# Optimization experiments

Measured on AMD Instinct MI355X. Metric: run time of the kernel, lower is better.

The kernel has to match this reference:

```python
import jax, jax.numpy as jnp
import numpy as np

EPS = 1e-10  # matches torch float32 path


def setup_inputs() -> dict:
    key = jax.random.key(0)
    ks = jax.random.split(key, 8)
    B, E, D, N = 32, 32000, 128, 1000
    scale = 1.0 / np.sqrt(D)
    return {
        "edge_attr": jax.random.normal(ks[0], (B, E, D), dtype=jnp.float32),
        "edge_index": jax.random.randint(ks[1], (B, 2, E), 0, N, dtype=jnp.int64),
        "W1": jax.random.normal(ks[2], (D, D), dtype=jnp.float32) * scale,
        "b1": jax.random.normal(ks[3], (D,), dtype=jnp.float32) * 0.01,
        "W2": jax.random.normal(ks[4], (D, D), dtype=jnp.float32) * scale,
        "b2": jax.random.normal(ks[5], (D,), dtype=jnp.float32) * 0.01,
        "Wout": jax.random.normal(ks[6], (1, D), dtype=jnp.float32) * scale,
        "bout": jax.random.normal(ks[7], (1,), dtype=jnp.float32) * 0.01,
        "num_nodes": N,
    }


def reference(edge_attr, edge_index, W1, b1, W2, b2, Wout, bout, num_nodes):
    # Edge MLP: (num_layers-1)=2 hidden silu linears, then 1-dim sigmoid output
    x = jax.nn.silu(jnp.einsum("bed,fd->bef", edge_attr, W1) + b1)
    x = jax.nn.silu(jnp.einsum("bed,fd->bef", x, W2) + b2)
    vals = jax.nn.sigmoid(jnp.einsum("bed,od->beo", x, Wout) + bout)[..., 0]  # [B, E]
    B = vals.shape[0]
    b_idx = jnp.arange(B)[:, None]  # [B, 1] broadcasts over E
    heatmap = jnp.zeros((B, num_nodes, num_nodes), dtype=vals.dtype)
    heatmap = heatmap.at[b_idx, edge_index[:, 0], edge_index[:, 1]].set(vals)
    return jnp.log(heatmap + EPS)
```

## Files before the change

kernel.cpp:

```cpp
#include <hip/hip_runtime.h>
#include <stdint.h>
#include <string.h>
#include <math.h>

typedef float f32x4 __attribute__((ext_vector_type(4)));
typedef unsigned int u32;

#define DD 128

__device__ __forceinline__ float fsilu(float x) {
    float e = __expf(-x);
    return x * __builtin_amdgcn_rcpf(1.0f + e);
}
__device__ __forceinline__ u32 pk4fp8(float a, float b, float c, float d) {
    u32 r = __builtin_amdgcn_cvt_pk_fp8_f32(a, b, 0u, false);
    return __builtin_amdgcn_cvt_pk_fp8_f32(c, d, r, true);
}

__device__ __forceinline__ float decz(u32 u) {
    float z = (float)(int)(u & 0x3FFFu) * (1.0f / 256.0f) - 40.0f;
    float s = __builtin_amdgcn_rcpf(1.0f + __expf(-z));
    return __logf(s + 1e-10f);
}
__global__ void decode_sparse(u32* __restrict__ p, long n4, u32 le) {
    long i  = (long)blockIdx.x * blockDim.x + threadIdx.x;
    long st = (long)gridDim.x * blockDim.x;
    for (long k = i; k < n4; k += st) {
        uint4 u = ((const uint4*)p)[k];
        float* f = (float*)(p + k * 4);
        if (u.x >= 0xE0000000u) f[0] = decz(u.x); else if (u.x != le) ((u32*)f)[0] = le;
        if (u.y >= 0xE0000000u) f[1] = decz(u.y); else if (u.y != le) ((u32*)f)[1] = le;
        if (u.z >= 0xE0000000u) f[2] = decz(u.z); else if (u.z != le) ((u32*)f)[2] = le;
        if (u.w >= 0xE0000000u) f[3] = decz(u.w); else if (u.w != le) ((u32*)f)[3] = le;
    }
}

__global__ __launch_bounds__(1024)
void mlp_scatter(const float* __restrict__ A,
                 const int* __restrict__ eidx,
                 const float* __restrict__ W1, const float* __restrict__ B1,
                 const float* __restrict__ W2, const float* __restrict__ B2,
                 const float* __restrict__ WO, const float* __restrict__ BO,
                 u32* __restrict__ out,
                 int E, int nWT, int N)
{
    extern __shared__ char smem[];
    uint2* W1s = (uint2*)smem;
    uint2* W2s = (uint2*)(smem + 16384);
    float* b1s = (float*)(smem + 32768);
    float* b2s = (float*)(smem + 33280);
    float* wos = (float*)(smem + 33792);
    uint2* Hs  = (uint2*)(smem + 34304);

    const int tid  = threadIdx.x;
    const int lane = tid & 63;
    const int wave = tid >> 6;
    const int lrow = lane & 15;
    const int lg   = lane >> 4;

    #pragma unroll
    for (int c = 0; c < 2; ++c) {
        int id = c * 1024 + tid;
        int mt = id >> 8, kk = (id >> 6) & 3, ln = id & 63;
        const float* p1 = W1 + (mt * 16 + (ln & 15)) * DD + kk * 32 + (ln >> 4) * 8;
        const float* p2 = W2 + (mt * 16 + (ln & 15)) * DD + kk * 32 + (ln >> 4) * 8;
        float4 x0 = *(const float4*)p1, x1 = *(const float4*)(p1 + 4);
        float4 y0 = *(const float4*)p2, y1 = *(const float4*)(p2 + 4);
        W1s[mt * 256 + kk * 64 + ln] = make_uint2(pk4fp8(x0.x, x0.y, x0.z, x0.w),
                                                  pk4fp8(x1.x, x1.y, x1.z, x1.w));
        W2s[mt * 256 + kk * 64 + ln] = make_uint2(pk4fp8(y0.x, y0.y, y0.z, y0.w),
                                                  pk4fp8(y1.x, y1.y, y1.z, y1.w));
    }
    if (tid < DD) { b1s[tid] = B1[tid]; b2s[tid] = B2[tid]; wos[tid] = WO[tid]; }
    const float bo = BO[0];
    const size_t NN = (size_t)N * (size_t)N;
    uint2* HsW = Hs + wave * 256;
    __syncthreads();

    const int wid  = blockIdx.x * 16 + wave;
    const int step = (int)gridDim.x * 16;
    if (wid >= nWT) return;

    float4 va[8];
    {
        const float* Ar = A + (size_t)((wid << 4) + lrow) * DD;
        #pragma unroll
        for (int kk = 0; kk < 4; ++kk) {
            const float* p = Ar + kk * 32 + lg * 8;
            va[2 * kk]     = *(const float4*)p;
            va[2 * kk + 1] = *(const float4*)(p + 4);
        }
    }

    for (int wt = wid; wt < nWT; wt += step) {
        const int r0  = wt << 4;
        const int b   = r0 / E;
        const int ei0 = r0 - b * E;
        int i0 = 0, j0 = 0;
        if (lane < 16) {
            i0 = eidx[(size_t)(2 * b) * E + ei0 + lane];
            j0 = eidx[(size_t)(2 * b + 1) * E + ei0 + lane];
        }

        uint2 ef[4];
        #pragma unroll
        for (int kk = 0; kk < 4; ++kk)
            ef[kk] = make_uint2(
                pk4fp8(va[2*kk].x,   va[2*kk].y,   va[2*kk].z,   va[2*kk].w),
                pk4fp8(va[2*kk+1].x, va[2*kk+1].y, va[2*kk+1].z, va[2*kk+1].w));

        {
            int tn = wt + step; if (tn >= nWT) tn = wt;
            const float* Ar = A + (size_t)((tn << 4) + lrow) * DD;
            #pragma unroll
            for (int kk = 0; kk < 4; ++kk) {
                const float* p = Ar + kk * 32 + lg * 8;
                va[2 * kk]     = *(const float4*)p;
                va[2 * kk + 1] = *(const float4*)(p + 4);
            }
        }

        f32x4 acc[8];
        #pragma unroll
        for (int mt = 0; mt < 8; ++mt)
            acc[mt] = *(const f32x4*)&b1s[mt * 16 + lg * 4];
        #pragma unroll
        for (int kk = 0; kk < 4; ++kk)
            #pragma unroll
            for (int mt = 0; mt < 8; ++mt)
                acc[mt] = __builtin_amdgcn_mfma_f32_16x16x32_fp8_fp8(
                    __builtin_bit_cast(long, W1s[mt * 256 + kk * 64 + lane]),
                    __builtin_bit_cast(long, ef[kk]), acc[mt], 0, 0, 0);

        #pragma unroll
        for (int mt = 0; mt < 8; ++mt) {
            int lnp = (((mt & 1) << 1) | (lg >> 1)) * 16 + lrow;
            u32 pw = pk4fp8(fsilu(acc[mt][0]), fsilu(acc[mt][1]),
                            fsilu(acc[mt][2]), fsilu(acc[mt][3]));
            ((u32*)&HsW[(mt >> 1) * 64 + lnp])[lg & 1] = pw;
        }

        f32x4 acc2[8];
        #pragma unroll
        for (int mt = 0; mt < 8; ++mt)
            acc2[mt] = *(const f32x4*)&b2s[mt * 16 + lg * 4];
        #pragma unroll
        for (int kk = 0; kk < 4; ++kk) {
            long hf = __builtin_bit_cast(long, HsW[kk * 64 + lane]);
            #pragma unroll
            for (int mt = 0; mt < 8; ++mt)
                acc2[mt] = __builtin_amdgcn_mfma_f32_16x16x32_fp8_fp8(
                    __builtin_bit_cast(long, W2s[mt * 256 + kk * 64 + lane]),
                    hf, acc2[mt], 0, 0, 0);
        }

        float zp = 0.f;
        #pragma unroll
        for (int mt = 0; mt < 8; ++mt) {
            f32x4 w4 = *(const f32x4*)&wos[mt * 16 + lg * 4];
            zp += w4[0] * fsilu(acc2[mt][0]) + w4[1] * fsilu(acc2[mt][1])
                + w4[2] * fsilu(acc2[mt][2]) + w4[3] * fsilu(acc2[mt][3]);
        }
        zp += __shfl_xor(zp, 16);
        zp += __shfl_xor(zp, 32);

        if (lane < 16) {
            float z = zp + bo;
            int qz = (int)((z + 40.0f) * 256.0f + 0.5f);
            qz = qz < 0 ? 0 : (qz > 16383 ? 16383 : qz);
            u32 packed = 0xE0000000u | ((u32)(ei0 + lane + 1) << 14) | (u32)qz;
            atomicMax(&out[(size_t)b * NN + (size_t)i0 * N + (size_t)j0], packed);
        }
    }
}

extern "C" void kernel_launch(void* const* d_in, const int* in_sizes, int n_in,
                              void* d_out, int out_size, void* d_ws, size_t ws_size,
                              hipStream_t stream) {
    const float* edge_attr  = (const float*)d_in[0];
    const int*   edge_index = (const int*)d_in[1];
    const float* W1   = (const float*)d_in[2];
    const float* b1   = (const float*)d_in[3];
    const float* W2   = (const float*)d_in[4];
    const float* b2   = (const float*)d_in[5];
    const float* Wout = (const float*)d_in[6];
    const float* bout = (const float*)d_in[7];

    long rows = (long)in_sizes[0] / DD;
    int  E    = in_sizes[1] / 64;
    int  nWT  = (int)(rows / 16);
    int  Bb   = (int)(rows / E);
    int  N    = (int)(sqrtf((float)(out_size / Bb)) + 0.5f);

    u32* outp = (u32*)d_out;
    long n4 = (long)out_size >> 2;

    float fv = logf(1e-10f);
    u32 LE; memcpy(&LE, &fv, 4);

    const int SMEM = 67072;
    hipFuncSetAttribute((const void*)mlp_scatter,
                        hipFuncAttributeMaxDynamicSharedMemorySize, SMEM);

    mlp_scatter<<<256, 1024, SMEM, stream>>>(edge_attr, edge_index, W1, b1, W2, b2,
                                             Wout, bout, outp, E, nWT, N);
    decode_sparse<<<2048, 256, 0, stream>>>(outp, n4, LE);
}
```

Before: 179.7 us.

## Shrink MLP blocks to 512 threads, drop register prefetch, reuse accumulators

Moves the fused MLP-scatter kernel from 256 blocks of 1024 threads to 768 blocks of 512 threads, cutting shared memory per block so more blocks can be resident per CU. It removes the software prefetch of the next tile's edge features held in registers and loads and packs the current tile directly. It also reuses the first-layer accumulator array for the second layer. The aim is lower register pressure and more waves in flight to hide memory latency, at the cost of exposing load latency that the prefetch used to hide and doing the weight staging more times across the larger grid.

```diff
diff --git a/kernel.cpp b/kernel.cpp
--- a/kernel.cpp
+++ b/kernel.cpp
@@ -35,7 +35,7 @@
     }
 }
 
-__global__ __launch_bounds__(1024)
+__global__ __launch_bounds__(512)
 void mlp_scatter(const float* __restrict__ A,
                  const int* __restrict__ eidx,
                  const float* __restrict__ W1, const float* __restrict__ B1,
@@ -59,8 +59,8 @@
     const int lg   = lane >> 4;
 
     #pragma unroll
-    for (int c = 0; c < 2; ++c) {
-        int id = c * 1024 + tid;
+    for (int c = 0; c < 4; ++c) {
+        int id = c * 512 + tid;
         int mt = id >> 8, kk = (id >> 6) & 3, ln = id & 63;
         const float* p1 = W1 + (mt * 16 + (ln & 15)) * DD + kk * 32 + (ln >> 4) * 8;
         const float* p2 = W2 + (mt * 16 + (ln & 15)) * DD + kk * 32 + (ln >> 4) * 8;
@@ -77,20 +77,8 @@
     uint2* HsW = Hs + wave * 256;
     __syncthreads();
 
-    const int wid  = blockIdx.x * 16 + wave;
-    const int step = (int)gridDim.x * 16;
-    if (wid >= nWT) return;
-
-    float4 va[8];
-    {
-        const float* Ar = A + (size_t)((wid << 4) + lrow) * DD;
-        #pragma unroll
-        for (int kk = 0; kk < 4; ++kk) {
-            const float* p = Ar + kk * 32 + lg * 8;
-            va[2 * kk]     = *(const float4*)p;
-            va[2 * kk + 1] = *(const float4*)(p + 4);
-        }
-    }
+    const int wid  = blockIdx.x * 8 + wave;
+    const int step = (int)gridDim.x * 8;
 
     for (int wt = wid; wt < nWT; wt += step) {
         const int r0  = wt << 4;
@@ -103,21 +91,24 @@
         }
 
         uint2 ef[4];
-        #pragma unroll
-        for (int kk = 0; kk < 4; ++kk)
-            ef[kk] = make_uint2(
-                pk4fp8(va[2*kk].x,   va[2*kk].y,   va[2*kk].z,   va[2*kk].w),
-                pk4fp8(va[2*kk+1].x, va[2*kk+1].y, va[2*kk+1].z, va[2*kk+1].w));
-
         {
-            int tn = wt + step; if (tn >= nWT) tn = wt;
-            const float* Ar = A + (size_t)((tn << 4) + lrow) * DD;
-            #pragma unroll
-            for (int kk = 0; kk < 4; ++kk) {
-                const float* p = Ar + kk * 32 + lg * 8;
-                va[2 * kk]     = *(const float4*)p;
-                va[2 * kk + 1] = *(const float4*)(p + 4);
-            }
+            const float* Ar = A + (size_t)(r0 + lrow) * DD + lg * 8;
+            float4 h0 = *(const float4*)(Ar);
+            float4 h1 = *(const float4*)(Ar + 4);
+            float4 h2 = *(const float4*)(Ar + 32);
+            float4 h3 = *(const float4*)(Ar + 36);
+            ef[0] = make_uint2(pk4fp8(h0.x, h0.y, h0.z, h0.w),
+                               pk4fp8(h1.x, h1.y, h1.z, h1.w));
+            ef[1] = make_uint2(pk4fp8(h2.x, h2.y, h2.z, h2.w),
+                               pk4fp8(h3.x, h3.y, h3.z, h3.w));
+            h0 = *(const float4*)(Ar + 64);
+            h1 = *(const float4*)(Ar + 68);
+            h2 = *(const float4*)(Ar + 96);
+            h3 = *(const float4*)(Ar + 100);
+            ef[2] = make_uint2(pk4fp8(h0.x, h0.y, h0.z, h0.w),
+                               pk4fp8(h1.x, h1.y, h1.z, h1.w));
+            ef[3] = make_uint2(pk4fp8(h2.x, h2.y, h2.z, h2.w),
+                               pk4fp8(h3.x, h3.y, h3.z, h3.w));
         }
 
         f32x4 acc[8];
@@ -140,26 +131,25 @@
             ((u32*)&HsW[(mt >> 1) * 64 + lnp])[lg & 1] = pw;
         }
 
-        f32x4 acc2[8];
         #pragma unroll
         for (int mt = 0; mt < 8; ++mt)
-            acc2[mt] = *(const f32x4*)&b2s[mt * 16 + lg * 4];
+            acc[mt] = *(const f32x4*)&b2s[mt * 16 + lg * 4];
         #pragma unroll
         for (int kk = 0; kk < 4; ++kk) {
             long hf = __builtin_bit_cast(long, HsW[kk * 64 + lane]);
             #pragma unroll
             for (int mt = 0; mt < 8; ++mt)
-                acc2[mt] = __builtin_amdgcn_mfma_f32_16x16x32_fp8_fp8(
+                acc[mt] = __builtin_amdgcn_mfma_f32_16x16x32_fp8_fp8(
                     __builtin_bit_cast(long, W2s[mt * 256 + kk * 64 + lane]),
-                    hf, acc2[mt], 0, 0, 0);
+                    hf, acc[mt], 0, 0, 0);
         }
 
         float zp = 0.f;
         #pragma unroll
         for (int mt = 0; mt < 8; ++mt) {
             f32x4 w4 = *(const f32x4*)&wos[mt * 16 + lg * 4];
-            zp += w4[0] * fsilu(acc2[mt][0]) + w4[1] * fsilu(acc2[mt][1])
-                + w4[2] * fsilu(acc2[mt][2]) + w4[3] * fsilu(acc2[mt][3]);
+            zp += w4[0] * fsilu(acc[mt][0]) + w4[1] * fsilu(acc[mt][1])
+                + w4[2] * fsilu(acc[mt][2]) + w4[3] * fsilu(acc[mt][3]);
         }
         zp += __shfl_xor(zp, 16);
         zp += __shfl_xor(zp, 32);
@@ -198,11 +188,11 @@
     float fv = logf(1e-10f);
     u32 LE; memcpy(&LE, &fv, 4);
 
-    const int SMEM = 67072;
+    const int SMEM = 50688;
     hipFuncSetAttribute((const void*)mlp_scatter,
                         hipFuncAttributeMaxDynamicSharedMemorySize, SMEM);
 
-    mlp_scatter<<<256, 1024, SMEM, stream>>>(edge_attr, edge_index, W1, b1, W2, b2,
-                                             Wout, bout, outp, E, nWT, N);
+    mlp_scatter<<<768, 512, SMEM, stream>>>(edge_attr, edge_index, W1, b1, W2, b2,
+                                            Wout, bout, outp, E, nWT, N);
     decode_sparse<<<2048, 256, 0, stream>>>(outp, n4, LE);
 }
```

After: 182.1 us. About the same (+1.3%).
